# Optimization experiments

Measured on AMD Instinct MI355X. Metric: run time of the kernel, lower is better.

Reference implementation:

```python
import jax, jax.numpy as jnp
import numpy as np

FACTOR = 2
MANUAL_PAD = 3


def make_kernel(k):
    k = jnp.asarray(k, dtype=jnp.float32)
    if k.ndim == 1:
        k = k[None, :] * k[:, None]
    return k / jnp.sum(k)


def setup_inputs() -> dict:
    key = jax.random.key(0)
    x = jax.random.normal(key, (8, 256, 128, 128), dtype=jnp.float32)
    # buffer: make_kernel([1,3,3,1]) * factor**2
    kernel = make_kernel([1.0, 3.0, 3.0, 1.0]) * (FACTOR ** 2)
    return {"x": x, "kernel": kernel}


def _circular_upsample(x, kernel):
    b, c, h, w = x.shape
    up = FACTOR
    mp = MANUAL_PAD
    kh, kw = kernel.shape
    p = kh - up
    pad0 = (p + 1) // 2 + up - 1  # = 2 for k=4, up=2
    pad1 = p // 2                 # = 1

    # manual circular padding (F.pad mode='circular')
    xp = jnp.pad(x, ((0, 0), (0, 0), (mp, mp), (mp, mp)), mode="wrap")
    hp, wp = h + 2 * mp, w + 2 * mp

    # upfirdn2d(up=factor, down=1, pad=(pad0,pad1)):
    # zero-insertion upsample + pad + TRUE convolution with the FIR kernel.
    # lhs_dilation performs the zero-insertion fused into the conv; dilated
    # length is H*up-(up-1), so add (up-1) trailing pad to match upfirdn's
    # H*up zero-inserted tensor. conv_general_dilated is a correlation, so
    # flip the kernel to realize true convolution.
    w_flip = jnp.flip(kernel)[None, None]  # (1,1,kh,kw)
    xr = xp.reshape(b * c, 1, hp, wp)      # depthwise: same filter per channel
    out = jax.lax.conv_general_dilated(
        xr, w_flip,
        window_strides=(1, 1),
        padding=((pad0, pad1 + up - 1), (pad0, pad1 + up - 1)),
        lhs_dilation=(up, up),
        dimension_numbers=("NCHW", "OIHW", "NCHW"),
    )
    oh, ow = out.shape[2], out.shape[3]  # = up*hp + pad0 + pad1 - kh + 1
    out = out.reshape(b, c, oh, ow)
    # final crop back to (up*h, up*w)
    return out[:, :, mp:up * h + mp, mp:up * w + mp]


def reference(x, kernel):
    return _circular_upsample(x, kernel)
```

## Files before the change

### kernel.cpp

```cpp
#include <hip/hip_runtime.h>


#define H 128
#define W 128
#define OH 256
#define OW 256

__global__ __launch_bounds__(256) void CircularUpsample2_kernel(
    const float* __restrict__ x, const float* __restrict__ k,
    float* __restrict__ out, int bc_count) {
  int idx = blockIdx.x * 256 + threadIdx.x;
  int t    = idx & 63;
  int rest = idx >> 6;
  int my   = rest & (H - 1);
  int bc   = rest >> 7;
  if (bc >= bc_count) return;

  const float* __restrict__ xp = x + (size_t)bc * (H * W);
  float* __restrict__ op = out + (size_t)bc * (OH * OW);

  int r0 = (my - 2) & (H - 1);
  int r1 = (my - 1) & (H - 1);
  int c0 = (2 * t - 2) & (W - 1);
  int c1 = (2 * t - 1) & (W - 1);
  int c2 = (2 * t) & (W - 1);

  float x00 = xp[r0 * W + c0], x01 = xp[r0 * W + c1], x02 = xp[r0 * W + c2];
  float x10 = xp[r1 * W + c0], x11 = xp[r1 * W + c1], x12 = xp[r1 * W + c2];

  float k00 = k[0],  k01 = k[1],  k02 = k[2],  k03 = k[3];
  float k10 = k[4],  k11 = k[5],  k12 = k[6],  k13 = k[7];
  float k20 = k[8],  k21 = k[9],  k22 = k[10], k23 = k[11];
  float k30 = k[12], k31 = k[13], k32 = k[14], k33 = k[15];

  float4 e;
  e.x = x00 * k22 + x01 * k20 + x10 * k02 + x11 * k00;
  e.y = x00 * k23 + x01 * k21 + x10 * k03 + x11 * k01;
  e.z = x01 * k22 + x02 * k20 + x11 * k02 + x12 * k00;
  e.w = x01 * k23 + x02 * k21 + x11 * k03 + x12 * k01;

  float4 o;
  o.x = x00 * k32 + x01 * k30 + x10 * k12 + x11 * k10;
  o.y = x00 * k33 + x01 * k31 + x10 * k13 + x11 * k11;
  o.z = x01 * k32 + x02 * k30 + x11 * k12 + x12 * k10;
  o.w = x01 * k33 + x02 * k31 + x11 * k13 + x12 * k11;

  *reinterpret_cast<float4*>(op + (size_t)(2 * my) * OW + 4 * t) = e;
  *reinterpret_cast<float4*>(op + (size_t)(2 * my + 1) * OW + 4 * t) = o;
}

extern "C" void kernel_launch(void* const* d_in, const int* in_sizes, int n_in,
                              void* d_out, int out_size, void* d_ws, size_t ws_size,
                              hipStream_t stream) {
  const float* x = (const float*)d_in[0];
  const float* k = (const float*)d_in[1];
  float* out = (float*)d_out;

  int bc_count = in_sizes[0] / (H * W);
  int total_threads = bc_count * (H) * (W / 2);
  int nblocks = (total_threads + 255) / 256;

  CircularUpsample2_kernel<<<nblocks, 256, 0, stream>>>(x, k, out, bc_count);
}
```

Before: 611.0 us.

## Widen per-thread work with vector loads, grid-stride loop and nontemporal stores

Each thread now produces eight output columns for an even and an odd row, using 128-bit vector loads of input rows instead of scalar loads. The launch becomes a fixed 2048-block grid-stride loop, so the filter weights are loaded once per thread and reused across iterations. Output writes use nontemporal stores to avoid cache pollution on a write-once stream. The risks are lower occupancy from higher register use and less parallelism with the fixed grid.

```diff
diff --git a/kernel.cpp b/kernel.cpp
--- a/kernel.cpp
+++ b/kernel.cpp
@@ -3,50 +3,58 @@
 
 #define H 128
 #define W 128
-#define OH 256
 #define OW 256
 
+using f32x4 = __attribute__((ext_vector_type(4))) float;
+
 __global__ __launch_bounds__(256) void CircularUpsample2_kernel(
-    const float* __restrict__ x, const float* __restrict__ k,
-    float* __restrict__ out, int bc_count) {
-  int idx = blockIdx.x * 256 + threadIdx.x;
-  int t    = idx & 63;
-  int rest = idx >> 6;
-  int my   = rest & (H - 1);
-  int bc   = rest >> 7;
-  if (bc >= bc_count) return;
+    const float* __restrict__ x, const float* __restrict__ kbuf,
+    float* __restrict__ out, int total_threads) {
+  float kw[16];
+#pragma unroll
+  for (int i = 0; i < 16; ++i) kw[i] = kbuf[i];
 
-  const float* __restrict__ xp = x + (size_t)bc * (H * W);
-  float* __restrict__ op = out + (size_t)bc * (OH * OW);
+  const int stride = gridDim.x * 256;
+  for (int idx = blockIdx.x * 256 + threadIdx.x; idx < total_threads; idx += stride) {
+    int s    = idx & 31;
+    int rest = idx >> 5;
+    int my   = rest & (H - 1);
+    int bc   = rest >> 7;
 
-  int r0 = (my - 2) & (H - 1);
-  int r1 = (my - 1) & (H - 1);
-  int c0 = (2 * t - 2) & (W - 1);
-  int c1 = (2 * t - 1) & (W - 1);
-  int c2 = (2 * t) & (W - 1);
+    const float* __restrict__ xp = x + (size_t)bc * (H * W);
+    float* __restrict__ op = out + (size_t)bc * (4 * H * W);
 
-  float x00 = xp[r0 * W + c0], x01 = xp[r0 * W + c1], x02 = xp[r0 * W + c2];
-  float x10 = xp[r1 * W + c0], x11 = xp[r1 * W + c1], x12 = xp[r1 * W + c2];
+    int r0 = (my - 2) & (H - 1);
+    int r1 = (my - 1) & (H - 1);
+    int ca = (4 * s - 4) & (W - 1);
+    int cb = 4 * s;
 
-  float k00 = k[0],  k01 = k[1],  k02 = k[2],  k03 = k[3];
-  float k10 = k[4],  k11 = k[5],  k12 = k[6],  k13 = k[7];
-  float k20 = k[8],  k21 = k[9],  k22 = k[10], k23 = k[11];
-  float k30 = k[12], k31 = k[13], k32 = k[14], k33 = k[15];
+    f32x4 a0 = *(const f32x4*)(xp + r0 * W + ca);
+    f32x4 a1 = *(const f32x4*)(xp + r0 * W + cb);
+    f32x4 b0 = *(const f32x4*)(xp + r1 * W + ca);
+    f32x4 b1 = *(const f32x4*)(xp + r1 * W + cb);
 
-  float4 e;
-  e.x = x00 * k22 + x01 * k20 + x10 * k02 + x11 * k00;
-  e.y = x00 * k23 + x01 * k21 + x10 * k03 + x11 * k01;
-  e.z = x01 * k22 + x02 * k20 + x11 * k02 + x12 * k00;
-  e.w = x01 * k23 + x02 * k21 + x11 * k03 + x12 * k01;
+    float u0[5] = {a0.z, a0.w, a1.x, a1.y, a1.z};
+    float u1[5] = {b0.z, b0.w, b1.x, b1.y, b1.z};
 
-  float4 o;
-  o.x = x00 * k32 + x01 * k30 + x10 * k12 + x11 * k10;
-  o.y = x00 * k33 + x01 * k31 + x10 * k13 + x11 * k11;
-  o.z = x01 * k32 + x02 * k30 + x11 * k12 + x12 * k10;
-  o.w = x01 * k33 + x02 * k31 + x11 * k13 + x12 * k11;
+    float ev[8], od[8];
+#pragma unroll
+    for (int j = 0; j < 8; ++j) {
+      int mxo = j >> 1, px = j & 1;
+      float A = u0[mxo], B = u0[mxo + 1], C = u1[mxo], D = u1[mxo + 1];
+      ev[j] = A * kw[10 + px] + B * kw[8 + px] + C * kw[2 + px] + D * kw[px];
+      od[j] = A * kw[14 + px] + B * kw[12 + px] + C * kw[6 + px] + D * kw[4 + px];
+    }
 
-  *reinterpret_cast<float4*>(op + (size_t)(2 * my) * OW + 4 * t) = e;
-  *reinterpret_cast<float4*>(op + (size_t)(2 * my + 1) * OW + 4 * t) = o;
+    float* pe = op + (size_t)(2 * my) * OW + 8 * s;
+    float* po = pe + OW;
+    f32x4 e0 = {ev[0], ev[1], ev[2], ev[3]}, e1 = {ev[4], ev[5], ev[6], ev[7]};
+    f32x4 o0 = {od[0], od[1], od[2], od[3]}, o1 = {od[4], od[5], od[6], od[7]};
+    __builtin_nontemporal_store(e0, (f32x4*)pe);
+    __builtin_nontemporal_store(e1, (f32x4*)(pe + 4));
+    __builtin_nontemporal_store(o0, (f32x4*)po);
+    __builtin_nontemporal_store(o1, (f32x4*)(po + 4));
+  }
 }
 
 extern "C" void kernel_launch(void* const* d_in, const int* in_sizes, int n_in,
@@ -57,8 +65,8 @@
   float* out = (float*)d_out;
 
   int bc_count = in_sizes[0] / (H * W);
-  int total_threads = bc_count * (H) * (W / 2);
-  int nblocks = (total_threads + 255) / 256;
+  int total_threads = bc_count * H * (W / 4);
+  int nblocks = 2048;
 
-  CircularUpsample2_kernel<<<nblocks, 256, 0, stream>>>(x, k, out, bc_count);
+  CircularUpsample2_kernel<<<nblocks, 256, 0, stream>>>(x, k, out, total_threads);
 }
```

Result: slower. 698.7 us (+14.4%).
